# Kernel tuning notes

Hardware: AMD Instinct MI355X
Metric: run time of the kernel (lower is better)

The kernel has to match this reference:

```python
import jax, jax.numpy as jnp
import numpy as np

N, D = 8192, 256
NEG_BIG = -9e15


def setup_inputs() -> dict:
    key = jax.random.key(0)
    k1, k2, k3 = jax.random.split(key, 3)
    h = jax.random.normal(k1, (N, D), dtype=jnp.float32)
    adj = jax.random.randint(k2, (N, N), 0, 2, dtype=jnp.int32)
    # xavier_uniform for a of shape (2D, 1): bound = sqrt(6/(2D+1))
    bound = np.sqrt(6.0 / (2 * D + 1)).astype(np.float32)
    a = jax.random.uniform(k3, (2 * D, 1), dtype=jnp.float32, minval=-bound, maxval=bound)
    return {"h": h, "adj": adj, "a": a}


def reference(h, adj, a):
    d = h.shape[1]
    h1 = h @ a[:d]            # [N, 1]
    h2 = h @ a[d:]            # [N, 1]
    e = jax.nn.leaky_relu(h1 + h2.T, negative_slope=0.01)  # [N, N]
    attention = jnp.where(adj > 0, e, NEG_BIG)
    attention = jax.nn.softmax(attention, axis=1)
    # dropout skipped: eval mode (training=False)
    return attention @ h      # [N, D]
```

## Files before the change

kernel.cpp:

```cpp
#include <hip/hip_runtime.h>
#include <hip/hip_bf16.h>

#define NTOT 8192
#define DDIM 256
#define ROWS 32
#define JWAVE 2048
#define NITER (JWAVE / 32)
#define NTSTR 131584
#define HTF_ELEMS (16 * NTSTR)

typedef __attribute__((ext_vector_type(8))) short short8;
typedef __attribute__((ext_vector_type(4))) float floatx4;
typedef __attribute__((ext_vector_type(4))) int intx4;

static __device__ __forceinline__ short bfp(float f) {
  __hip_bfloat16 b = __float2bfloat16(f);
  return *(short*)&b;
}

__global__ __launch_bounds__(256) void gat_scores(const float* __restrict__ h,
                                                  const float* __restrict__ a,
                                                  float2* __restrict__ rc,
                                                  float2* __restrict__ etab) {
  int row  = blockIdx.x * 4 + (threadIdx.x >> 6);
  int lane = threadIdx.x & 63;
  const float* hr = h + (size_t)row * DDIM;
  float p1 = 0.f, p2 = 0.f;
#pragma unroll
  for (int k = 0; k < DDIM / 64; ++k) {
    int idx  = lane + 64 * k;
    float hv = hr[idx];
    p1 += hv * a[idx];
    p2 += hv * a[DDIM + idx];
  }
#pragma unroll
  for (int off = 32; off > 0; off >>= 1) {
    p1 += __shfl_down(p1, off, 64);
    p2 += __shfl_down(p2, off, 64);
  }
  if (lane == 0) {
    rc[row]   = make_float2(__expf(p1), __expf(0.01f * p1));
    etab[row] = make_float2(__expf(p2), __expf(0.01f * p2));
  }
}

__global__ __launch_bounds__(256) void gat_hpack(const float* __restrict__ h,
                                                 ushort* __restrict__ hTf) {
  __shared__ float tile[64][257];
  const int t    = threadIdx.x;
  const int lane = t & 63;
  const int w    = t >> 6;
  const int quad = lane >> 4;
  const int c    = lane & 15;
  const int i0   = blockIdx.x * 64;

#pragma unroll
  for (int it = 0; it < 16; ++it) {
    int r = it * 4 + w;
    float4 v = *(const float4*)(h + (size_t)(i0 + r) * DDIM + lane * 4);
    tile[r][lane * 4 + 0] = v.x; tile[r][lane * 4 + 1] = v.y;
    tile[r][lane * 4 + 2] = v.z; tile[r][lane * 4 + 3] = v.w;
  }
  __syncthreads();

#pragma unroll
  for (int k = 0; k < 4; ++k) {
    const int n = 4 * k + w;
#pragma unroll
    for (int jbl = 0; jbl < 2; ++jbl) {
      short8 vv;
#pragma unroll
      for (int i = 0; i < 8; ++i) {
        float f = tile[jbl * 32 + quad * 8 + i][n * 16 + c];
        vv[i] = bfp(f);
      }
      *(short8*)(hTf + ((size_t)(n * 257 + i0 / 32 + jbl) * 64 + lane) * 8) = vv;
    }
  }
}

__global__ __launch_bounds__(1024, 4) void gat_attn(const ushort* __restrict__ hTf,
                                                    const int* __restrict__ adj,
                                                    const float2* __restrict__ rc,
                                                    const float2* __restrict__ etab,
                                                    float* __restrict__ out) {
  __shared__ float slab[8][32][64];
  __shared__ float lsum[4][32];

  const int t    = threadIdx.x;
  const int lane = t & 63;
  const int w    = t >> 6;
  const int quad = lane >> 4;
  const int c    = lane & 15;
  const int rg   = w & 1;
  const int cg   = (w >> 1) & 1;
  const int jg   = w >> 2;
  const int r0   = blockIdx.x * ROWS;
  const int rb   = r0 + rg * 16;
  const int j0   = jg * JWAVE;

  const float2 rcv = rc[rb + c];
  const float E1 = rcv.x, E2 = rcv.y;

  const int*    ap  = adj + (size_t)(rb + c) * NTOT + j0 + quad * 8;
  const float*  etb = (const float*)(etab + j0 + quad * 8);
  const ushort* hb  = hTf + (size_t)(8 * cg) * NTSTR + (size_t)(j0 / 32) * 512 + lane * 8;

  floatx4 acc[8];
#pragma unroll
  for (int q = 0; q < 8; ++q) acc[q] = (floatx4){0.f, 0.f, 0.f, 0.f};

  float lp = 0.f;
  short8 bA[4], bB[4];
  intx4  aj0, aj1;
  float4 ea, eb, ec, ed;

  #define LDA(jt)                                                              \
    {                                                                          \
      const int* p_ = ap + (size_t)(jt) * 32;                                  \
      aj0 = __builtin_nontemporal_load((const intx4*)p_);                      \
      aj1 = __builtin_nontemporal_load((const intx4*)(p_ + 4));                \
    }
  #define LDE(jt)                                                              \
    {                                                                          \
      const float* e_ = etb + (size_t)(jt) * 64;                               \
      ea = ((const float4*)e_)[0];                                             \
      eb = ((const float4*)e_)[1];                                             \
      ec = ((const float4*)e_)[2];                                             \
      ed = ((const float4*)e_)[3];                                             \
    }
  #define LDBA(jt)                                                             \
    _Pragma("unroll")                                                          \
    for (int q = 0; q < 4; ++q)                                                \
      bA[q] = *(const short8*)(hb + (size_t)(jt) * 512 + (size_t)q * NTSTR);
  #define LDBB(jt)                                                             \
    _Pragma("unroll")                                                          \
    for (int q = 0; q < 4; ++q)                                                \
      bB[q] = *(const short8*)(hb + (size_t)(jt) * 512 + (size_t)(4 + q) * NTSTR);

  LDBA(0)
  LDBB(0)
  LDA(0)
  LDE(0)

  for (int jt = 0; jt < NITER; ++jt) {
    const int jn = (jt + 1) & (NITER - 1);

    const int   am[8] = {aj0[0], aj0[1], aj0[2], aj0[3], aj1[0], aj1[1], aj1[2], aj1[3]};
    const float tp[16] = {ea.x, ea.y, ea.z, ea.w, eb.x, eb.y, eb.z, eb.w,
                          ec.x, ec.y, ec.z, ec.w, ed.x, ed.y, ed.z, ed.w};
    short8 pa;
#pragma unroll
    for (int i = 0; i < 8; ++i) {
      const float p = (am[i] > 0) ? fmaxf(E1 * tp[2 * i], E2 * tp[2 * i + 1]) : 0.f;
      lp += p;
      pa[i] = bfp(p);
    }

    LDA(jn)
    LDE(jn)
    __builtin_amdgcn_sched_barrier(0);

#pragma unroll
    for (int q = 0; q < 4; ++q)
      acc[q] = __builtin_amdgcn_mfma_f32_16x16x32_bf16(pa, bA[q], acc[q], 0, 0, 0);
    LDBA(jn)
    __builtin_amdgcn_sched_barrier(0);

#pragma unroll
    for (int q = 0; q < 4; ++q)
      acc[4 + q] = __builtin_amdgcn_mfma_f32_16x16x32_bf16(pa, bB[q], acc[4 + q], 0, 0, 0);
    LDBB(jn)
    __builtin_amdgcn_sched_barrier(0);
  }
  #undef LDA
  #undef LDE
  #undef LDBA
  #undef LDBB

  lp += __shfl_xor(lp, 16, 64);
  lp += __shfl_xor(lp, 32, 64);
  if (cg == 0 && lane < 16) lsum[jg][rg * 16 + lane] = lp;

  const int sidx = rg * 2 + cg;
  if (jg >= 2) {
#pragma unroll
    for (int q = 0; q < 8; ++q)
#pragma unroll
      for (int r = 0; r < 4; ++r)
        slab[(jg - 2) * 4 + sidx][q * 4 + r][lane] = acc[q][r];
  }
  __syncthreads();
  if (jg < 2) {
#pragma unroll
    for (int q = 0; q < 8; ++q)
#pragma unroll
      for (int r = 0; r < 4; ++r)
        acc[q][r] += slab[jg * 4 + sidx][q * 4 + r][lane];
  }
  __syncthreads();
  if (jg == 1) {
#pragma unroll
    for (int q = 0; q < 8; ++q)
#pragma unroll
      for (int r = 0; r < 4; ++r)
        slab[sidx][q * 4 + r][lane] = acc[q][r];
  }
  __syncthreads();
  if (jg == 0) {
    float linv[4];
#pragma unroll
    for (int r = 0; r < 4; ++r) {
      const int lr = rg * 16 + quad * 4 + r;
      linv[r] = 1.f / (lsum[0][lr] + lsum[1][lr] + lsum[2][lr] + lsum[3][lr]);
    }
#pragma unroll
    for (int q = 0; q < 8; ++q)
#pragma unroll
      for (int r = 0; r < 4; ++r) {
        float v = acc[q][r] + slab[sidx][q * 4 + r][lane];
        __builtin_nontemporal_store(
            v * linv[r],
            &out[(size_t)(rb + quad * 4 + r) * DDIM + cg * 128 + q * 16 + c]);
      }
  }
}

extern "C" void kernel_launch(void* const* d_in, const int* in_sizes, int n_in,
                              void* d_out, int out_size, void* d_ws, size_t ws_size,
                              hipStream_t stream) {
  const float* h   = (const float*)d_in[0];
  const int*   adj = (const int*)d_in[1];
  const float* a   = (const float*)d_in[2];
  float* out = (float*)d_out;

  float2*   rc    = (float2*)d_ws;
  float2*   etab  = rc + NTOT;
  ushort*   hTf   = (ushort*)(etab + NTOT);

  gat_scores<<<NTOT / 4, 256, 0, stream>>>(h, a, rc, etab);
  gat_hpack<<<NTOT / 64, 256, 0, stream>>>(h, hTf);
  gat_attn<<<NTOT / ROWS, 1024, 0, stream>>>(hTf, adj, rc, etab, out);
}
```

Measured before the change: 519.7 us.

## Split attention key dimension across XCD-mapped blocks with partial-sum combine kernel

Result: slower. 550.2 us (+5.9%).

```diff
diff --git a/kernel.cpp b/kernel.cpp
--- a/kernel.cpp
+++ b/kernel.cpp
@@ -4,7 +4,9 @@
 #define NTOT 8192
 #define DDIM 256
 #define ROWS 32
-#define JWAVE 2048
+#define NXCD 8
+#define JSLICE (NTOT / NXCD)
+#define JWAVE (JSLICE / 4)
 #define NITER (JWAVE / 32)
 #define NTSTR 131584
 #define HTF_ELEMS (16 * NTSTR)
@@ -83,7 +85,8 @@
                                                     const int* __restrict__ adj,
                                                     const float2* __restrict__ rc,
                                                     const float2* __restrict__ etab,
-                                                    float* __restrict__ out) {
+                                                    float* __restrict__ pout,
+                                                    float* __restrict__ plp) {
   __shared__ float slab[8][32][64];
   __shared__ float lsum[4][32];
 
@@ -95,9 +98,11 @@
   const int rg   = w & 1;
   const int cg   = (w >> 1) & 1;
   const int jg   = w >> 2;
-  const int r0   = blockIdx.x * ROWS;
+  const int js   = blockIdx.x & (NXCD - 1);
+  const int rt   = blockIdx.x >> 3;
+  const int r0   = rt * ROWS;
   const int rb   = r0 + rg * 16;
-  const int j0   = jg * JWAVE;
+  const int j0   = js * JSLICE + jg * JWAVE;
 
   const float2 rcv = rc[rb + c];
   const float E1 = rcv.x, E2 = rcv.y;
@@ -208,22 +213,41 @@
   }
   __syncthreads();
   if (jg == 0) {
-    float linv[4];
-#pragma unroll
-    for (int r = 0; r < 4; ++r) {
-      const int lr = rg * 16 + quad * 4 + r;
-      linv[r] = 1.f / (lsum[0][lr] + lsum[1][lr] + lsum[2][lr] + lsum[3][lr]);
-    }
+    float* pob = pout + (size_t)js * NTOT * DDIM;
 #pragma unroll
     for (int q = 0; q < 8; ++q)
 #pragma unroll
       for (int r = 0; r < 4; ++r) {
         float v = acc[q][r] + slab[sidx][q * 4 + r][lane];
         __builtin_nontemporal_store(
-            v * linv[r],
-            &out[(size_t)(rb + quad * 4 + r) * DDIM + cg * 128 + q * 16 + c]);
+            v, &pob[(size_t)(rb + quad * 4 + r) * DDIM + cg * 128 + q * 16 + c]);
       }
-  }
+    if (cg == 0 && lane < 16) {
+      const int lr = rg * 16 + lane;
+      plp[(size_t)js * NTOT + r0 + lr] =
+          lsum[0][lr] + lsum[1][lr] + lsum[2][lr] + lsum[3][lr];
+    }
+  }
+}
+
+__global__ __launch_bounds__(256) void gat_combine(const float* __restrict__ pout,
+                                                   const float* __restrict__ plp,
+                                                   float* __restrict__ out) {
+  const int idx = blockIdx.x * 256 + threadIdx.x;
+  const int row = idx >> 6;
+  float4 s = make_float4(0.f, 0.f, 0.f, 0.f);
+  float d = 0.f;
+#pragma unroll
+  for (int js = 0; js < NXCD; ++js) {
+    float4 v = ((const float4*)(pout + (size_t)js * NTOT * DDIM))[idx];
+    s.x += v.x; s.y += v.y; s.z += v.z; s.w += v.w;
+    d += plp[(size_t)js * NTOT + row];
+  }
+  const float inv = 1.f / d;
+  __builtin_nontemporal_store(s.x * inv, &out[idx * 4 + 0]);
+  __builtin_nontemporal_store(s.y * inv, &out[idx * 4 + 1]);
+  __builtin_nontemporal_store(s.z * inv, &out[idx * 4 + 2]);
+  __builtin_nontemporal_store(s.w * inv, &out[idx * 4 + 3]);
 }
 
 extern "C" void kernel_launch(void* const* d_in, const int* in_sizes, int n_in,
@@ -237,8 +261,11 @@
   float2*   rc    = (float2*)d_ws;
   float2*   etab  = rc + NTOT;
   ushort*   hTf   = (ushort*)(etab + NTOT);
+  float*    pout  = (float*)(hTf + HTF_ELEMS);
+  float*    plp   = pout + (size_t)NXCD * NTOT * DDIM;
 
   gat_scores<<<NTOT / 4, 256, 0, stream>>>(h, a, rc, etab);
   gat_hpack<<<NTOT / 64, 256, 0, stream>>>(h, hTf);
-  gat_attn<<<NTOT / ROWS, 1024, 0, stream>>>(hTf, adj, rc, etab, out);
-}
+  gat_attn<<<NXCD * (NTOT / ROWS), 1024, 0, stream>>>(hTf, adj, rc, etab, pout, plp);
+  gat_combine<<<(NTOT * DDIM / 4) / 256, 256, 0, stream>>>(pout, plp, out);
+}
```

## Pack adjacency into transposed bitmask and restructure attention waves over row tiles

Applied to the files above, without the earlier changes.

Measured after the change: 472.6 us. -9.1%, faster.

```diff
diff --git a/kernel.cpp b/kernel.cpp
--- a/kernel.cpp
+++ b/kernel.cpp
@@ -6,6 +6,7 @@
 #define ROWS 32
 #define JWAVE 2048
 #define NITER (JWAVE / 32)
+#define NWORDS (NTOT / 32)
 #define NTSTR 131584
 #define HTF_ELEMS (16 * NTSTR)
 
@@ -41,6 +42,39 @@
   if (lane == 0) {
     rc[row]   = make_float2(__expf(p1), __expf(0.01f * p1));
     etab[row] = make_float2(__expf(p2), __expf(0.01f * p2));
+  }
+}
+
+__global__ __launch_bounds__(256) void gat_pack(const int* __restrict__ adj,
+                                                unsigned* __restrict__ bitsT) {
+  __shared__ unsigned words[64][65];
+  const int t    = threadIdx.x;
+  const int lane = t & 63;
+  const int w    = t >> 6;
+  const int r0   = blockIdx.x * 64;
+  const int jb   = blockIdx.y * 2048;
+
+#pragma unroll 2
+  for (int rr = 0; rr < 16; ++rr) {
+    const int rl = w * 16 + rr;
+    const int* ap = adj + (size_t)(r0 + rl) * NTOT + jb + lane * 4;
+#pragma unroll
+    for (int R = 0; R < 8; ++R) {
+      intx4 v = __builtin_nontemporal_load((const intx4*)(ap + R * 256));
+      unsigned nib = (v[0] > 0 ? 1u : 0u) | (v[1] > 0 ? 2u : 0u) |
+                     (v[2] > 0 ? 4u : 0u) | (v[3] > 0 ? 8u : 0u);
+      unsigned b8  = nib | (__shfl_xor((int)nib, 1, 64) << 4);
+      unsigned b16 = b8  | (__shfl_xor((int)b8,  2, 64) << 8);
+      unsigned b32 = b16 | (__shfl_xor((int)b16, 4, 64) << 16);
+      if ((lane & 7) == 0) words[rl][R * 8 + (lane >> 3)] = b32;
+    }
+  }
+  __syncthreads();
+
+#pragma unroll 4
+  for (int kk = 0; kk < 16; ++kk) {
+    const int jwl = w * 16 + kk;
+    bitsT[(size_t)(jb / 32 + jwl) * NTOT + r0 + lane] = words[lane][jwl];
   }
 }
 
@@ -80,7 +114,7 @@
 }
 
 __global__ __launch_bounds__(1024, 4) void gat_attn(const ushort* __restrict__ hTf,
-                                                    const int* __restrict__ adj,
+                                                    const unsigned* __restrict__ bitsT,
                                                     const float2* __restrict__ rc,
                                                     const float2* __restrict__ etab,
                                                     float* __restrict__ out) {
@@ -92,34 +126,36 @@
   const int w    = t >> 6;
   const int quad = lane >> 4;
   const int c    = lane & 15;
-  const int rg   = w & 1;
-  const int cg   = (w >> 1) & 1;
+  const int cg   = w & 3;
   const int jg   = w >> 2;
   const int r0   = blockIdx.x * ROWS;
-  const int rb   = r0 + rg * 16;
   const int j0   = jg * JWAVE;
 
-  const float2 rcv = rc[rb + c];
-  const float E1 = rcv.x, E2 = rcv.y;
-
-  const int*    ap  = adj + (size_t)(rb + c) * NTOT + j0 + quad * 8;
-  const float*  etb = (const float*)(etab + j0 + quad * 8);
-  const ushort* hb  = hTf + (size_t)(8 * cg) * NTSTR + (size_t)(j0 / 32) * 512 + lane * 8;
-
-  floatx4 acc[8];
-#pragma unroll
-  for (int q = 0; q < 8; ++q) acc[q] = (floatx4){0.f, 0.f, 0.f, 0.f};
-
-  float lp = 0.f;
-  short8 bA[4], bB[4];
-  intx4  aj0, aj1;
+  const float2 rc0 = rc[r0 + c];
+  const float2 rc1 = rc[r0 + 16 + c];
+  const float E10 = rc0.x, E20 = rc0.y;
+  const float E11 = rc1.x, E21 = rc1.y;
+
+  const unsigned* mb  = bitsT + (size_t)(j0 / 32) * NTOT + r0;
+  const float*    etb = (const float*)(etab + j0 + quad * 8);
+  const ushort*   hb  = hTf + (size_t)(cg * 4) * NTSTR + (size_t)(j0 / 32) * 512 + lane * 8;
+
+  floatx4 acc[2][4];
+#pragma unroll
+  for (int rt = 0; rt < 2; ++rt)
+#pragma unroll
+    for (int q = 0; q < 4; ++q) acc[rt][q] = (floatx4){0.f, 0.f, 0.f, 0.f};
+
+  float lp0 = 0.f, lp1 = 0.f;
+  short8 bD[4];
+  unsigned W0, W1;
   float4 ea, eb, ec, ed;
 
-  #define LDA(jt)                                                              \
+  #define LDM(jt)                                                              \
     {                                                                          \
-      const int* p_ = ap + (size_t)(jt) * 32;                                  \
-      aj0 = __builtin_nontemporal_load((const intx4*)p_);                      \
-      aj1 = __builtin_nontemporal_load((const intx4*)(p_ + 4));                \
+      const unsigned* m_ = mb + (size_t)(jt) * NTOT;                           \
+      W0 = m_[c];                                                              \
+      W1 = m_[16 + c];                                                         \
     }
   #define LDE(jt)                                                              \
     {                                                                          \
@@ -129,100 +165,116 @@
       ec = ((const float4*)e_)[2];                                             \
       ed = ((const float4*)e_)[3];                                             \
     }
-  #define LDBA(jt)                                                             \
-    _Pragma("unroll")                                                          \
-    for (int q = 0; q < 4; ++q)                                                \
-      bA[q] = *(const short8*)(hb + (size_t)(jt) * 512 + (size_t)q * NTSTR);
-  #define LDBB(jt)                                                             \
-    _Pragma("unroll")                                                          \
-    for (int q = 0; q < 4; ++q)                                                \
-      bB[q] = *(const short8*)(hb + (size_t)(jt) * 512 + (size_t)(4 + q) * NTSTR);
-
-  LDBA(0)
-  LDBB(0)
-  LDA(0)
+  #define LDB01(jt)                                                            \
+    bD[0] = *(const short8*)(hb + (size_t)(jt) * 512);                         \
+    bD[1] = *(const short8*)(hb + (size_t)(jt) * 512 + NTSTR);
+  #define LDB23(jt)                                                            \
+    bD[2] = *(const short8*)(hb + (size_t)(jt) * 512 + 2 * (size_t)NTSTR);     \
+    bD[3] = *(const short8*)(hb + (size_t)(jt) * 512 + 3 * (size_t)NTSTR);
+
+  LDB01(0)
+  LDB23(0)
+  LDM(0)
   LDE(0)
 
   for (int jt = 0; jt < NITER; ++jt) {
     const int jn = (jt + 1) & (NITER - 1);
 
-    const int   am[8] = {aj0[0], aj0[1], aj0[2], aj0[3], aj1[0], aj1[1], aj1[2], aj1[3]};
+    const unsigned bm0 = (W0 >> (quad * 8)) & 0xff;
+    const unsigned bm1 = (W1 >> (quad * 8)) & 0xff;
     const float tp[16] = {ea.x, ea.y, ea.z, ea.w, eb.x, eb.y, eb.z, eb.w,
                           ec.x, ec.y, ec.z, ec.w, ed.x, ed.y, ed.z, ed.w};
-    short8 pa;
+    short8 pa0, pa1;
 #pragma unroll
     for (int i = 0; i < 8; ++i) {
-      const float p = (am[i] > 0) ? fmaxf(E1 * tp[2 * i], E2 * tp[2 * i + 1]) : 0.f;
-      lp += p;
-      pa[i] = bfp(p);
-    }
-
-    LDA(jn)
+      const float t1 = tp[2 * i], t2 = tp[2 * i + 1];
+      const float m  = fmaxf(E10 * t1, E20 * t2);
+      const float n  = fmaxf(E11 * t1, E21 * t2);
+      const float p0 = ((bm0 >> i) & 1u) ? m : 0.f;
+      const float p1 = ((bm1 >> i) & 1u) ? n : 0.f;
+      lp0 += p0; lp1 += p1;
+      pa0[i] = bfp(p0);
+      pa1[i] = bfp(p1);
+    }
+
+    LDM(jn)
     LDE(jn)
     __builtin_amdgcn_sched_barrier(0);
 
-#pragma unroll
-    for (int q = 0; q < 4; ++q)
-      acc[q] = __builtin_amdgcn_mfma_f32_16x16x32_bf16(pa, bA[q], acc[q], 0, 0, 0);
-    LDBA(jn)
+    acc[0][0] = __builtin_amdgcn_mfma_f32_16x16x32_bf16(pa0, bD[0], acc[0][0], 0, 0, 0);
+    acc[1][0] = __builtin_amdgcn_mfma_f32_16x16x32_bf16(pa1, bD[0], acc[1][0], 0, 0, 0);
+    acc[0][1] = __builtin_amdgcn_mfma_f32_16x16x32_bf16(pa0, bD[1], acc[0][1], 0, 0, 0);
+    acc[1][1] = __builtin_amdgcn_mfma_f32_16x16x32_bf16(pa1, bD[1], acc[1][1], 0, 0, 0);
+    LDB01(jn)
     __builtin_amdgcn_sched_barrier(0);
 
-#pragma unroll
-    for (int q = 0; q < 4; ++q)
-      acc[4 + q] = __builtin_amdgcn_mfma_f32_16x16x32_bf16(pa, bB[q], acc[4 + q], 0, 0, 0);
-    LDBB(jn)
+    acc[0][2] = __builtin_amdgcn_mfma_f32_16x16x32_bf16(pa0, bD[2], acc[0][2], 0, 0, 0);
+    acc[1][2] = __builtin_amdgcn_mfma_f32_16x16x32_bf16(pa1, bD[2], acc[1][2], 0, 0, 0);
+    acc[0][3] = __builtin_amdgcn_mfma_f32_16x16x32_bf16(pa0, bD[3], acc[0][3], 0, 0, 0);
+    acc[1][3] = __builtin_amdgcn_mfma_f32_16x16x32_bf16(pa1, bD[3], acc[1][3], 0, 0, 0);
+    LDB23(jn)
     __builtin_amdgcn_sched_barrier(0);
   }
-  #undef LDA
+  #undef LDM
   #undef LDE
-  #undef LDBA
-  #undef LDBB
-
-  lp += __shfl_xor(lp, 16, 64);
-  lp += __shfl_xor(lp, 32, 64);
-  if (cg == 0 && lane < 16) lsum[jg][rg * 16 + lane] = lp;
-
-  const int sidx = rg * 2 + cg;
+  #undef LDB01
+  #undef LDB23
+
+  lp0 += __shfl_xor(lp0, 16, 64); lp0 += __shfl_xor(lp0, 32, 64);
+  lp1 += __shfl_xor(lp1, 16, 64); lp1 += __shfl_xor(lp1, 32, 64);
+  if (cg == 0 && lane < 16) { lsum[jg][lane] = lp0; lsum[jg][16 + lane] = lp1; }
+
   if (jg >= 2) {
 #pragma unroll
-    for (int q = 0; q < 8; ++q)
-#pragma unroll
-      for (int r = 0; r < 4; ++r)
-        slab[(jg - 2) * 4 + sidx][q * 4 + r][lane] = acc[q][r];
+    for (int rt = 0; rt < 2; ++rt)
+#pragma unroll
+      for (int q = 0; q < 4; ++q)
+#pragma unroll
+        for (int r = 0; r < 4; ++r)
+          slab[(jg - 2) * 4 + cg][rt * 16 + quad * 4 + r][q * 16 + c] = acc[rt][q][r];
   }
   __syncthreads();
   if (jg < 2) {
 #pragma unroll
-    for (int q = 0; q < 8; ++q)
-#pragma unroll
-      for (int r = 0; r < 4; ++r)
-        acc[q][r] += slab[jg * 4 + sidx][q * 4 + r][lane];
+    for (int rt = 0; rt < 2; ++rt)
+#pragma unroll
+      for (int q = 0; q < 4; ++q)
+#pragma unroll
+        for (int r = 0; r < 4; ++r)
+          acc[rt][q][r] += slab[jg * 4 + cg][rt * 16 + quad * 4 + r][q * 16 + c];
   }
   __syncthreads();
   if (jg == 1) {
 #pragma unroll
-    for (int q = 0; q < 8; ++q)
-#pragma unroll
-      for (int r = 0; r < 4; ++r)
-        slab[sidx][q * 4 + r][lane] = acc[q][r];
+    for (int rt = 0; rt < 2; ++rt)
+#pragma unroll
+      for (int q = 0; q < 4; ++q)
+#pragma unroll
+        for (int r = 0; r < 4; ++r)
+          slab[cg][rt * 16 + quad * 4 + r][q * 16 + c] = acc[rt][q][r];
   }
   __syncthreads();
   if (jg == 0) {
-    float linv[4];
-#pragma unroll
-    for (int r = 0; r < 4; ++r) {
-      const int lr = rg * 16 + quad * 4 + r;
-      linv[r] = 1.f / (lsum[0][lr] + lsum[1][lr] + lsum[2][lr] + lsum[3][lr]);
-    }
-#pragma unroll
-    for (int q = 0; q < 8; ++q)
+    float linv[2][4];
+#pragma unroll
+    for (int rt = 0; rt < 2; ++rt)
 #pragma unroll
       for (int r = 0; r < 4; ++r) {
-        float v = acc[q][r] + slab[sidx][q * 4 + r][lane];
-        __builtin_nontemporal_store(
-            v * linv[r],
-            &out[(size_t)(rb + quad * 4 + r) * DDIM + cg * 128 + q * 16 + c]);
+        const int lr = rt * 16 + quad * 4 + r;
+        linv[rt][r] = 1.f / (lsum[0][lr] + lsum[1][lr] + lsum[2][lr] + lsum[3][lr]);
       }
+#pragma unroll
+    for (int rt = 0; rt < 2; ++rt)
+#pragma unroll
+      for (int q = 0; q < 4; ++q)
+#pragma unroll
+        for (int r = 0; r < 4; ++r) {
+          float v = acc[rt][q][r] + slab[cg][rt * 16 + quad * 4 + r][q * 16 + c];
+          __builtin_nontemporal_store(
+              v * linv[rt][r],
+              &out[(size_t)(r0 + rt * 16 + quad * 4 + r) * DDIM +
+                   (cg * 4 + q) * 16 + c]);
+        }
   }
 }
 
@@ -236,9 +288,11 @@
 
   float2*   rc    = (float2*)d_ws;
   float2*   etab  = rc + NTOT;
-  ushort*   hTf   = (ushort*)(etab + NTOT);
+  unsigned* bitsT = (unsigned*)(etab + NTOT);
+  ushort*   hTf   = (ushort*)(bitsT + (size_t)NWORDS * NTOT);
 
   gat_scores<<<NTOT / 4, 256, 0, stream>>>(h, a, rc, etab);
+  gat_pack<<<dim3(NTOT / 64, 4), 256, 0, stream>>>(adj, bitsT);
   gat_hpack<<<NTOT / 64, 256, 0, stream>>>(h, hTf);
-  gat_attn<<<NTOT / ROWS, 1024, 0, stream>>>(hTf, adj, rc, etab, out);
-}
+  gat_attn<<<NTOT / ROWS, 1024, 0, stream>>>(hTf, bitsT, rc, etab, out);
+}
```

## Process 64 rows per wave to reuse h fragments, split j across blocks

Applied to the files above, without the earlier changes.

New measurement: 455.8 us. 12.3% less time.

```diff
diff --git a/kernel.cpp b/kernel.cpp
--- a/kernel.cpp
+++ b/kernel.cpp
@@ -3,8 +3,10 @@
 
 #define NTOT 8192
 #define DDIM 256
-#define ROWS 32
-#define JWAVE 2048
+#define ROWS 64
+#define JSPL 2
+#define JBLK (NTOT / JSPL)
+#define JWAVE (JBLK / 4)
 #define NITER (JWAVE / 32)
 #define NTSTR 131584
 #define HTF_ELEMS (16 * NTSTR)
@@ -79,48 +81,58 @@
   }
 }
 
-__global__ __launch_bounds__(1024, 4) void gat_attn(const ushort* __restrict__ hTf,
-                                                    const int* __restrict__ adj,
-                                                    const float2* __restrict__ rc,
-                                                    const float2* __restrict__ etab,
-                                                    float* __restrict__ out) {
-  __shared__ float slab[8][32][64];
-  __shared__ float lsum[4][32];
+__global__ __launch_bounds__(512, 2) void gat_attn(const ushort* __restrict__ hTf,
+                                                   const int* __restrict__ adj,
+                                                   const float2* __restrict__ rc,
+                                                   const float2* __restrict__ etab,
+                                                   float* __restrict__ pout,
+                                                   float* __restrict__ plp) {
+  __shared__ float slab[4][64][64];
+  __shared__ float lsum[4][64];
 
   const int t    = threadIdx.x;
   const int lane = t & 63;
   const int w    = t >> 6;
   const int quad = lane >> 4;
   const int c    = lane & 15;
-  const int rg   = w & 1;
-  const int cg   = (w >> 1) & 1;
-  const int jg   = w >> 2;
+  const int cg   = w & 1;
+  const int jg   = w >> 1;
   const int r0   = blockIdx.x * ROWS;
-  const int rb   = r0 + rg * 16;
-  const int j0   = jg * JWAVE;
-
-  const float2 rcv = rc[rb + c];
-  const float E1 = rcv.x, E2 = rcv.y;
-
-  const int*    ap  = adj + (size_t)(rb + c) * NTOT + j0 + quad * 8;
+  const int jb   = blockIdx.y;
+  const int j0   = jb * JBLK + jg * JWAVE;
+
+  const float2 rv0 = rc[r0 + c];
+  const float2 rv1 = rc[r0 + 16 + c];
+  const float2 rv2 = rc[r0 + 32 + c];
+  const float2 rv3 = rc[r0 + 48 + c];
+
+  const int* ap0 = adj + (size_t)(r0 + c) * NTOT + j0 + quad * 8;
+  const int* ap1 = ap0 + (size_t)16 * NTOT;
+  const int* ap2 = ap0 + (size_t)32 * NTOT;
+  const int* ap3 = ap0 + (size_t)48 * NTOT;
   const float*  etb = (const float*)(etab + j0 + quad * 8);
-  const ushort* hb  = hTf + (size_t)(8 * cg) * NTSTR + (size_t)(j0 / 32) * 512 + lane * 8;
-
-  floatx4 acc[8];
-#pragma unroll
-  for (int q = 0; q < 8; ++q) acc[q] = (floatx4){0.f, 0.f, 0.f, 0.f};
-
-  float lp = 0.f;
-  short8 bA[4], bB[4];
-  intx4  aj0, aj1;
+  const ushort* hb  = hTf + (size_t)(cg * 8) * NTSTR + (size_t)(j0 / 32) * 512 + lane * 8;
+
+  floatx4 acc[4][8];
+#pragma unroll
+  for (int f = 0; f < 4; ++f)
+#pragma unroll
+    for (int q = 0; q < 8; ++q) acc[f][q] = (floatx4){0.f, 0.f, 0.f, 0.f};
+
+  float lp0 = 0.f, lp1 = 0.f, lp2 = 0.f, lp3 = 0.f;
+  short8 bD[8];
+  intx4 a0a, a0b, a1a, a1b, a2a, a2b, a3a, a3b;
   float4 ea, eb, ec, ed;
 
   #define LDA(jt)                                                              \
-    {                                                                          \
-      const int* p_ = ap + (size_t)(jt) * 32;                                  \
-      aj0 = __builtin_nontemporal_load((const intx4*)p_);                      \
-      aj1 = __builtin_nontemporal_load((const intx4*)(p_ + 4));                \
-    }
+    a0a = __builtin_nontemporal_load((const intx4*)(ap0 + (size_t)(jt) * 32)); \
+    a0b = __builtin_nontemporal_load((const intx4*)(ap0 + (size_t)(jt) * 32 + 4)); \
+    a1a = __builtin_nontemporal_load((const intx4*)(ap1 + (size_t)(jt) * 32)); \
+    a1b = __builtin_nontemporal_load((const intx4*)(ap1 + (size_t)(jt) * 32 + 4)); \
+    a2a = __builtin_nontemporal_load((const intx4*)(ap2 + (size_t)(jt) * 32)); \
+    a2b = __builtin_nontemporal_load((const intx4*)(ap2 + (size_t)(jt) * 32 + 4)); \
+    a3a = __builtin_nontemporal_load((const intx4*)(ap3 + (size_t)(jt) * 32)); \
+    a3b = __builtin_nontemporal_load((const intx4*)(ap3 + (size_t)(jt) * 32 + 4));
   #define LDE(jt)                                                              \
     {                                                                          \
       const float* e_ = etb + (size_t)(jt) * 64;                               \
@@ -129,101 +141,165 @@
       ec = ((const float4*)e_)[2];                                             \
       ed = ((const float4*)e_)[3];                                             \
     }
-  #define LDBA(jt)                                                             \
-    _Pragma("unroll")                                                          \
-    for (int q = 0; q < 4; ++q)                                                \
-      bA[q] = *(const short8*)(hb + (size_t)(jt) * 512 + (size_t)q * NTSTR);
-  #define LDBB(jt)                                                             \
-    _Pragma("unroll")                                                          \
-    for (int q = 0; q < 4; ++q)                                                \
-      bB[q] = *(const short8*)(hb + (size_t)(jt) * 512 + (size_t)(4 + q) * NTSTR);
-
-  LDBA(0)
-  LDBB(0)
+  #define LDB03(jt)                                                            \
+    bD[0] = *(const short8*)(hb + (size_t)(jt) * 512);                         \
+    bD[1] = *(const short8*)(hb + (size_t)(jt) * 512 + (size_t)1 * NTSTR);     \
+    bD[2] = *(const short8*)(hb + (size_t)(jt) * 512 + (size_t)2 * NTSTR);     \
+    bD[3] = *(const short8*)(hb + (size_t)(jt) * 512 + (size_t)3 * NTSTR);
+  #define LDB47(jt)                                                            \
+    bD[4] = *(const short8*)(hb + (size_t)(jt) * 512 + (size_t)4 * NTSTR);     \
+    bD[5] = *(const short8*)(hb + (size_t)(jt) * 512 + (size_t)5 * NTSTR);     \
+    bD[6] = *(const short8*)(hb + (size_t)(jt) * 512 + (size_t)6 * NTSTR);     \
+    bD[7] = *(const short8*)(hb + (size_t)(jt) * 512 + (size_t)7 * NTSTR);
+
+  #define PB(AA, AB, RV, PAF, LPF)                                             \
+    {                                                                          \
+      const int am[8] = {AA[0], AA[1], AA[2], AA[3], AB[0], AB[1], AB[2], AB[3]}; \
+      _Pragma("unroll")                                                        \
+      for (int i = 0; i < 8; ++i) {                                            \
+        const float p = (am[i] > 0)                                            \
+            ? fmaxf(RV.x * tp[2 * i], RV.y * tp[2 * i + 1]) : 0.f;             \
+        LPF += p;                                                              \
+        PAF[i] = bfp(p);                                                       \
+      }                                                                        \
+    }
+
+  LDB03(0)
+  LDB47(0)
   LDA(0)
   LDE(0)
 
   for (int jt = 0; jt < NITER; ++jt) {
     const int jn = (jt + 1) & (NITER - 1);
 
-    const int   am[8] = {aj0[0], aj0[1], aj0[2], aj0[3], aj1[0], aj1[1], aj1[2], aj1[3]};
     const float tp[16] = {ea.x, ea.y, ea.z, ea.w, eb.x, eb.y, eb.z, eb.w,
                           ec.x, ec.y, ec.z, ec.w, ed.x, ed.y, ed.z, ed.w};
-    short8 pa;
-#pragma unroll
-    for (int i = 0; i < 8; ++i) {
-      const float p = (am[i] > 0) ? fmaxf(E1 * tp[2 * i], E2 * tp[2 * i + 1]) : 0.f;
-      lp += p;
-      pa[i] = bfp(p);
-    }
+    short8 pa0, pa1, pa2, pa3;
+    PB(a0a, a0b, rv0, pa0, lp0)
+    PB(a1a, a1b, rv1, pa1, lp1)
+    PB(a2a, a2b, rv2, pa2, lp2)
+    PB(a3a, a3b, rv3, pa3, lp3)
 
     LDA(jn)
     LDE(jn)
     __builtin_amdgcn_sched_barrier(0);
 
 #pragma unroll
-    for (int q = 0; q < 4; ++q)
-      acc[q] = __builtin_amdgcn_mfma_f32_16x16x32_bf16(pa, bA[q], acc[q], 0, 0, 0);
-    LDBA(jn)
+    for (int q = 0; q < 4; ++q) {
+      acc[0][q] = __builtin_amdgcn_mfma_f32_16x16x32_bf16(pa0, bD[q], acc[0][q], 0, 0, 0);
+      acc[1][q] = __builtin_amdgcn_mfma_f32_16x16x32_bf16(pa1, bD[q], acc[1][q], 0, 0, 0);
+      acc[2][q] = __builtin_amdgcn_mfma_f32_16x16x32_bf16(pa2, bD[q], acc[2][q], 0, 0, 0);
+      acc[3][q] = __builtin_amdgcn_mfma_f32_16x16x32_bf16(pa3, bD[q], acc[3][q], 0, 0, 0);
+    }
+    LDB03(jn)
     __builtin_amdgcn_sched_barrier(0);
 
 #pragma unroll
-    for (int q = 0; q < 4; ++q)
-      acc[4 + q] = __builtin_amdgcn_mfma_f32_16x16x32_bf16(pa, bB[q], acc[4 + q], 0, 0, 0);
-    LDBB(jn)
+    for (int q = 4; q < 8; ++q) {
+      acc[0][q] = __builtin_amdgcn_mfma_f32_16x16x32_bf16(pa0, bD[q], acc[0][q], 0, 0, 0);
+      acc[1][q] = __builtin_amdgcn_mfma_f32_16x16x32_bf16(pa1, bD[q], acc[1][q], 0, 0, 0);
+      acc[2][q] = __builtin_amdgcn_mfma_f32_16x16x32_bf16(pa2, bD[q], acc[2][q], 0, 0, 0);
+      acc[3][q] = __builtin_amdgcn_mfma_f32_16x16x32_bf16(pa3, bD[q], acc[3][q], 0, 0, 0);
+    }
+    LDB47(jn)
     __builtin_amdgcn_sched_barrier(0);
   }
   #undef LDA
   #undef LDE
-  #undef LDBA
-  #undef LDBB
-
-  lp += __shfl_xor(lp, 16, 64);
-  lp += __shfl_xor(lp, 32, 64);
-  if (cg == 0 && lane < 16) lsum[jg][rg * 16 + lane] = lp;
-
-  const int sidx = rg * 2 + cg;
-  if (jg >= 2) {
-#pragma unroll
-    for (int q = 0; q < 8; ++q)
-#pragma unroll
-      for (int r = 0; r < 4; ++r)
-        slab[(jg - 2) * 4 + sidx][q * 4 + r][lane] = acc[q][r];
-  }
-  __syncthreads();
-  if (jg < 2) {
-#pragma unroll
-    for (int q = 0; q < 8; ++q)
-#pragma unroll
-      for (int r = 0; r < 4; ++r)
-        acc[q][r] += slab[jg * 4 + sidx][q * 4 + r][lane];
-  }
-  __syncthreads();
-  if (jg == 1) {
-#pragma unroll
-    for (int q = 0; q < 8; ++q)
-#pragma unroll
-      for (int r = 0; r < 4; ++r)
-        slab[sidx][q * 4 + r][lane] = acc[q][r];
-  }
-  __syncthreads();
-  if (jg == 0) {
-    float linv[4];
-#pragma unroll
-    for (int r = 0; r < 4; ++r) {
-      const int lr = rg * 16 + quad * 4 + r;
-      linv[r] = 1.f / (lsum[0][lr] + lsum[1][lr] + lsum[2][lr] + lsum[3][lr]);
-    }
-#pragma unroll
-    for (int q = 0; q < 8; ++q)
-#pragma unroll
-      for (int r = 0; r < 4; ++r) {
-        float v = acc[q][r] + slab[sidx][q * 4 + r][lane];
-        __builtin_nontemporal_store(
-            v * linv[r],
-            &out[(size_t)(rb + quad * 4 + r) * DDIM + cg * 128 + q * 16 + c]);
-      }
-  }
+  #undef LDB03
+  #undef LDB47
+  #undef PB
+
+  lp0 += __shfl_xor(lp0, 16, 64); lp0 += __shfl_xor(lp0, 32, 64);
+  lp1 += __shfl_xor(lp1, 16, 64); lp1 += __shfl_xor(lp1, 32, 64);
+  lp2 += __shfl_xor(lp2, 16, 64); lp2 += __shfl_xor(lp2, 32, 64);
+  lp3 += __shfl_xor(lp3, 16, 64); lp3 += __shfl_xor(lp3, 32, 64);
+  if (cg == 0 && lane < 16) {
+    lsum[jg][lane]      = lp0;
+    lsum[jg][16 + lane] = lp1;
+    lsum[jg][32 + lane] = lp2;
+    lsum[jg][48 + lane] = lp3;
+  }
+
+  float* pob = pout + (size_t)jb * NTOT * DDIM;
+#pragma unroll
+  for (int hd = 0; hd < 2; ++hd) {
+    if (jg >= 2) {
+#pragma unroll
+      for (int f = 0; f < 4; ++f)
+#pragma unroll
+        for (int qq = 0; qq < 4; ++qq)
+#pragma unroll
+          for (int r = 0; r < 4; ++r)
+            slab[(jg - 2) * 2 + cg][f * 16 + quad * 4 + r][qq * 16 + c] =
+                acc[f][hd * 4 + qq][r];
+    }
+    __syncthreads();
+    if (jg < 2) {
+#pragma unroll
+      for (int f = 0; f < 4; ++f)
+#pragma unroll
+        for (int qq = 0; qq < 4; ++qq)
+#pragma unroll
+          for (int r = 0; r < 4; ++r)
+            acc[f][hd * 4 + qq][r] +=
+                slab[jg * 2 + cg][f * 16 + quad * 4 + r][qq * 16 + c];
+    }
+    __syncthreads();
+    if (jg == 1) {
+#pragma unroll
+      for (int f = 0; f < 4; ++f)
+#pragma unroll
+        for (int qq = 0; qq < 4; ++qq)
+#pragma unroll
+          for (int r = 0; r < 4; ++r)
+            slab[cg][f * 16 + quad * 4 + r][qq * 16 + c] = acc[f][hd * 4 + qq][r];
+    }
+    __syncthreads();
+    if (jg == 0) {
+#pragma unroll
+      for (int f = 0; f < 4; ++f)
+#pragma unroll
+        for (int qq = 0; qq < 4; ++qq)
+#pragma unroll
+          for (int r = 0; r < 4; ++r) {
+            float v = acc[f][hd * 4 + qq][r] +
+                      slab[cg][f * 16 + quad * 4 + r][qq * 16 + c];
+            __builtin_nontemporal_store(
+                v, &pob[(size_t)(r0 + f * 16 + quad * 4 + r) * DDIM +
+                        cg * 128 + hd * 64 + qq * 16 + c]);
+          }
+    }
+    __syncthreads();
+  }
+
+  if (jg == 0 && cg == 0 && lane < 16) {
+#pragma unroll
+    for (int f = 0; f < 4; ++f) {
+      const int lr = f * 16 + lane;
+      plp[(size_t)jb * NTOT + r0 + lr] =
+          lsum[0][lr] + lsum[1][lr] + lsum[2][lr] + lsum[3][lr];
+    }
+  }
+}
+
+__global__ __launch_bounds__(256) void gat_combine(const float* __restrict__ pout,
+                                                   const float* __restrict__ plp,
+                                                   float* __restrict__ out) {
+  const int idx = blockIdx.x * 256 + threadIdx.x;
+  const int row = idx >> 6;
+  float4 a = ((const float4*)pout)[idx];
+  float4 b = ((const float4*)(pout + (size_t)NTOT * DDIM))[idx];
+  float inv = 1.f / (plp[row] + plp[NTOT + row]);
+  float4 r;
+  r.x = (a.x + b.x) * inv;
+  r.y = (a.y + b.y) * inv;
+  r.z = (a.z + b.z) * inv;
+  r.w = (a.w + b.w) * inv;
+  __builtin_nontemporal_store(r.x, &out[idx * 4 + 0]);
+  __builtin_nontemporal_store(r.y, &out[idx * 4 + 1]);
+  __builtin_nontemporal_store(r.z, &out[idx * 4 + 2]);
+  __builtin_nontemporal_store(r.w, &out[idx * 4 + 3]);
 }
 
 extern "C" void kernel_launch(void* const* d_in, const int* in_sizes, int n_in,
@@ -237,8 +313,11 @@
   float2*   rc    = (float2*)d_ws;
   float2*   etab  = rc + NTOT;
   ushort*   hTf   = (ushort*)(etab + NTOT);
+  float*    pout  = (float*)(hTf + HTF_ELEMS);
+  float*    plp   = pout + (size_t)JSPL * NTOT * DDIM;
 
   gat_scores<<<NTOT / 4, 256, 0, stream>>>(h, a, rc, etab);
   gat_hpack<<<NTOT / 64, 256, 0, stream>>>(h, hTf);
-  gat_attn<<<NTOT / ROWS, 1024, 0, stream>>>(hTf, adj, rc, etab, out);
-}
+  gat_attn<<<dim3(NTOT / ROWS, JSPL), 512, 0, stream>>>(hTf, adj, rc, etab, pout, plp);
+  gat_combine<<<(NTOT * DDIM / 4) / 256, 256, 0, stream>>>(pout, plp, out);
+}
```
